# Kernel tuning notes

Hardware: AMD Instinct MI355X
Metric: run time of the kernel (lower is better)

The kernel has to match this reference:

```python
import jax, jax.numpy as jnp
import numpy as np

P_DIMS = [512, 256, 128]
K_DIMS = [256, 256, 256]
NT = 65536


def setup_inputs() -> dict:
    key = jax.random.key(0)
    ks = jax.random.split(key, 8 * len(P_DIMS))
    inp = {}
    ki = 0
    for i, (p, k) in enumerate(zip(P_DIMS, K_DIMS)):
        inp[f"x{i}"] = jax.random.normal(ks[ki], (NT, p), jnp.float32); ki += 1
        inp[f"alpha{i}"] = jax.random.normal(ks[ki], (1, k), jnp.float32); ki += 1
        inp[f"beta{i}"] = jax.random.normal(ks[ki], (k, p), jnp.float32) * 0.05; ki += 1
        inp[f"sig{i}"] = jax.random.normal(ks[ki], (1, k), jnp.float32); ki += 1
        inp[f"eta{i}"] = jax.random.normal(ks[ki], (1, k), jnp.float32); ki += 1
        inp[f"gam{i}"] = jax.random.normal(ks[ki], (k, 1), jnp.float32) * 0.03; ki += 1
        inp[f"w{i}"] = jax.random.normal(ks[ki], (k, p), jnp.float32); ki += 1
        inp[f"disc{i}"] = jnp.array([3.0], jnp.float32); ki += 1
    return inp


def _source(x, alpha, beta, sig, eta, gam, w, disc):
    # x: (nt,p); w,beta: (k,p); alpha,sig,eta: (1,k); gam: (k,1); disc: (1,)
    h = eta ** 2                                           # (1,k)
    d2 = (jnp.sum(x * x, axis=1, keepdims=True)
          - 2.0 * (x @ w.T)
          + jnp.sum(w * w, axis=1)[None, :])
    a = jnp.exp(-(gam[:, 0] ** 2)[None, :] * d2)           # (nt,k)
    ah = a * h                                             # a * H
    hx = jnp.sum(ah, axis=1)                               # (nt,)
    mu = x @ beta.T + alpha                                # (nt,k)
    mux = jnp.sum(mu * ah, axis=1) / hx
    sig2x = jnp.sum((sig ** 2) * (ah ** 2), axis=1) / (hx * hx)
    hx_dc = hx * jax.nn.sigmoid(disc[0])
    return mux, sig2x, hx, hx_dc


def reference(x0, alpha0, beta0, sig0, eta0, gam0, w0, disc0,
              x1, alpha1, beta1, sig1, eta1, gam1, w1, disc1,
              x2, alpha2, beta2, sig2, eta2, gam2, w2, disc2):
    srcs = [
        (x0, alpha0, beta0, sig0, eta0, gam0, w0, disc0),
        (x1, alpha1, beta1, sig1, eta1, gam1, w1, disc1),
        (x2, alpha2, beta2, sig2, eta2, gam2, w2, disc2),
    ]
    outs = [_source(*s) for s in srcs]  # fixed small loop over sources
    mux_t = jnp.stack([o[0] for o in outs])     # (S,nt)
    sig2x_t = jnp.stack([o[1] for o in outs])
    hx_t = jnp.stack([o[2] for o in outs])
    hx_dc = jnp.stack([o[3] for o in outs])
    denom = jnp.sum(hx_dc, axis=0)
    mux_comb = jnp.sum(mux_t * hx_dc, axis=0) / denom
    sig2x_comb = jnp.sum(sig2x_t * hx_dc ** 2, axis=0) / (denom ** 2)
    mux_final = jnp.concatenate([mux_t, mux_comb[None]], axis=0)      # (S+1,nt)
    sig2x_final = jnp.concatenate([sig2x_t, sig2x_comb[None]], axis=0)
    hx_final = jnp.concatenate([hx_t, denom[None]], axis=0)
    return (mux_final, sig2x_final, hx_final)
```

## Files before the change

kernel.cpp:

```cpp
#include <hip/hip_runtime.h>
#include <hip/hip_bf16.h>

typedef __attribute__((ext_vector_type(8))) short short8;
typedef __attribute__((ext_vector_type(4))) float f32x4;

#define NT 65536

__device__ __forceinline__ unsigned short f2bf(float f) {
    union { float f; unsigned int u; } v; v.f = f;
    unsigned int u = v.u;
    unsigned int r = (u + 0x7fffu + ((u >> 16) & 1u)) >> 16;
    return (unsigned short)r;
}

__device__ __forceinline__ unsigned int cvt_pk_bf16(float lo, float hi) {
    unsigned int r;
    asm("v_cvt_pk_bf16_f32 %0, %1, %2" : "=v"(r) : "v"(lo), "v"(hi));
    return r;
}

#define LGKM0()  asm volatile("s_waitcnt lgkmcnt(0)" ::: "memory")
#define BAR()    __builtin_amdgcn_s_barrier()
#define SB0()    __builtin_amdgcn_sched_barrier(0)

__global__ void prep_kernel(const float* __restrict__ w0, const float* __restrict__ b0,
                            const float* __restrict__ a0, const float* __restrict__ s0,
                            const float* __restrict__ e0, const float* __restrict__ g0,
                            const float* __restrict__ w1, const float* __restrict__ b1,
                            const float* __restrict__ a1, const float* __restrict__ s1,
                            const float* __restrict__ e1, const float* __restrict__ g1,
                            const float* __restrict__ w2, const float* __restrict__ b2,
                            const float* __restrict__ a2, const float* __restrict__ s2,
                            const float* __restrict__ e2, const float* __restrict__ g2,
                            unsigned short* __restrict__ bc, float* __restrict__ prmAll) {
    __shared__ float red[2];
    const int bx = blockIdx.x;
    const int s = bx >> 9;
    const int n = bx & 511;
    const int P = 512 >> s;
    const float* w   = (s == 0) ? w0 : ((s == 1) ? w1 : w2);
    const float* bet = (s == 0) ? b0 : ((s == 1) ? b1 : b2);
    const float* alp = (s == 0) ? a0 : ((s == 1) ? a1 : a2);
    const float* sig = (s == 0) ? s0 : ((s == 1) ? s1 : s2);
    const float* eta = (s == 0) ? e0 : ((s == 1) ? e1 : e2);
    const float* gam = (s == 0) ? g0 : ((s == 1) ? g1 : g2);
    unsigned short* dstb = bc + ((s == 0) ? 0 : ((s == 1) ? (512 * 512) : (512 * 512 + 512 * 256)));
    float* prm = prmAll + 1280 * s;

    const int tid = threadIdx.x;
    const int k16 = n >> 5;
    const int typ = (n >> 4) & 1;
    const int k = k16 * 16 + (n & 15);
    const bool isw = (typ == 0);
    const float* src = (isw ? w : bet) + (size_t)k * P;
    unsigned short* dst = dstb + (size_t)n * P;
    float ss = 0.f;
    for (int c = tid; c < P; c += 128) {
        float f = src[c];
        dst[c] = f2bf(f);
        if (isw) ss += f * f;
    }
#pragma unroll
    for (int m = 1; m < 64; m <<= 1) ss += __shfl_xor(ss, m);
    if ((tid & 63) == 0) red[tid >> 6] = ss;
    __syncthreads();
    if (isw && tid == 0) prm[k] = red[0] + red[1];
    if (n == 0) {
        for (int kk = tid; kk < 256; kk += 128) {
            float g = gam[kk], e = eta[kk];
            prm[256 + kk]  = g * g;
            prm[512 + kk]  = e * e;
            prm[768 + kk]  = alp[kk];
            prm[1024 + kk] = sig[kk] * sig[kk];
        }
    }
}

template<int P>
__global__ __launch_bounds__(256, 3)
void fused_src(const float* __restrict__ x, const unsigned short* __restrict__ Bc,
               const float* __restrict__ prm, float* __restrict__ pwsS) {
    constexpr int NK = P / 32;
    __shared__ unsigned short Bs[4][128 * 32];
    __shared__ unsigned short Xs[2][128 * 32];
    __shared__ float xn2[128];

    const int b = blockIdx.x;
    const int xt = (b >> 5) * 8 + (b & 7);
    const int pt = (b >> 3) & 3;

    const int tid = threadIdx.x, lane = tid & 63, wv = tid >> 6;
    const int wp = wv >> 1, wx = wv & 1;
    const int l15 = lane & 15, l4 = lane >> 4;

    const int srow = tid >> 1, shalf = tid & 1;
    const float* xbase = x + (size_t)(xt * 128 + srow) * P + shalf * 16;

    f32x4 acc[4][4];
#pragma unroll
    for (int pf = 0; pf < 4; pf++)
#pragma unroll
        for (int xf = 0; xf < 4; xf++) acc[pf][xf] = (f32x4){0.f, 0.f, 0.f, 0.f};

    float4 xr[4][4];
    float ss = 0.f;

    auto gloadB = [&](int nb, int t) {
#pragma unroll
        for (int i = 0; i < 2; i++) {
            const int u = i * 256 + tid;
            const int row = u >> 2;
            const int sl = (u & 3) ^ ((row >> 1) & 3);
            const unsigned short* src = Bc + (size_t)(pt * 128 + row) * P + t * 32 + sl * 8;
            __builtin_amdgcn_global_load_lds((const __attribute__((address_space(1))) void*)src,
                (__attribute__((address_space(3))) void*)&Bs[nb][(i * 256 + wv * 64) * 8], 16, 0, 0);
        }
    };
    auto loadX = [&](float4* xrs, int t) {
#pragma unroll
        for (int i = 0; i < 4; i++) xrs[i] = *(const float4*)(xbase + t * 32 + i * 4);
    };
    auto cvtWrite = [&](const float4* xrs, int xb) {
        const int sw = (srow >> 1) & 3;
#pragma unroll
        for (int hh = 0; hh < 2; hh++) {
            float4 q0 = xrs[2 * hh], q1 = xrs[2 * hh + 1];
            ss += q0.x*q0.x + q0.y*q0.y + q0.z*q0.z + q0.w*q0.w
                + q1.x*q1.x + q1.y*q1.y + q1.z*q1.z + q1.w*q1.w;
            uint4 pk = { cvt_pk_bf16(q0.x, q0.y), cvt_pk_bf16(q0.z, q0.w),
                         cvt_pk_bf16(q1.x, q1.y), cvt_pk_bf16(q1.z, q1.w) };
            const int phys = (shalf * 2 + hh) ^ sw;
            *(uint4*)(&Xs[xb][srow * 32 + phys * 8]) = pk;
        }
    };
    auto compute = [&](int bb, int xb) {
        short8 af[4], bf[4];
#pragma unroll
        for (int pf = 0; pf < 4; pf++) {
            const int row = 64 * wp + 16 * pf + l15;
            af[pf] = *(const short8*)(&Bs[bb][row * 32 + ((l4 ^ ((row >> 1) & 3)) << 3)]);
        }
#pragma unroll
        for (int xf = 0; xf < 4; xf++) {
            const int row = 64 * wx + 16 * xf + l15;
            bf[xf] = *(const short8*)(&Xs[xb][row * 32 + ((l4 ^ ((row >> 1) & 3)) << 3)]);
        }
#pragma unroll
        for (int pf = 0; pf < 4; pf++)
#pragma unroll
            for (int xf = 0; xf < 4; xf++)
                acc[pf][xf] = __builtin_amdgcn_mfma_f32_16x16x32_bf16(af[pf], bf[xf], acc[pf][xf], 0, 0, 0);
    };

#pragma unroll
    for (int d = 0; d < 3; d++) {
        if (d < NK) {
            gloadB(d, d); SB0();
            loadX(xr[d], d); SB0();
        }
    }
    cvtWrite(xr[0], 0);
    LGKM0(); SB0(); BAR(); SB0();

#pragma unroll
    for (int t = 0; t < NK; t++) {
        if (t + 3 < NK) {
            gloadB((t + 3) & 3, t + 3); SB0();
            loadX(xr[(t + 3) & 3], t + 3); SB0();
        }
        if (t + 1 < NK) {
            cvtWrite(xr[(t + 1) & 3], (t + 1) & 1);
        }
        LGKM0(); SB0(); BAR(); SB0();
        compute(t & 3, t & 1);
        SB0(); BAR(); SB0();
    }

    ss += __shfl_xor(ss, 1);
    if (shalf == 0) xn2[srow] = ss;
    __syncthreads();

    const int kb0 = (pt * 4 + 2 * wp) * 16 + 4 * l4;
    f32x4 wn2[2], g2[2], hv[2], alv[2], s2v[2];
#pragma unroll
    for (int K = 0; K < 2; K++) {
        const int kk = kb0 + 16 * K;
        wn2[K] = *(const f32x4*)(prm + kk);
        g2[K]  = *(const f32x4*)(prm + 256 + kk);
        hv[K]  = *(const f32x4*)(prm + 512 + kk);
        alv[K] = *(const f32x4*)(prm + 768 + kk);
        s2v[K] = *(const f32x4*)(prm + 1024 + kk);
    }
    float (*part)[128][3] = (float (*)[128][3])(&Bs[0][0]);
#pragma unroll
    for (int xf = 0; xf < 4; xf++) {
        const int xrow = 64 * wx + 16 * xf + l15;
        const float xv = xn2[xrow];
        float hs = 0.f, ms = 0.f, gs = 0.f;
#pragma unroll
        for (int K = 0; K < 2; K++) {
#pragma unroll
            for (int j = 0; j < 4; j++) {
                const float aw = acc[2 * K][xf][j];
                const float ab = acc[2 * K + 1][xf][j];
                const float d2 = xv - 2.f * aw + wn2[K][j];
                const float a  = __expf(-g2[K][j] * d2);
                const float ah = a * hv[K][j];
                hs += ah;
                ms += (ab + alv[K][j]) * ah;
                gs += s2v[K][j] * ah * ah;
            }
        }
        hs += __shfl_xor(hs, 16); hs += __shfl_xor(hs, 32);
        ms += __shfl_xor(ms, 16); ms += __shfl_xor(ms, 32);
        gs += __shfl_xor(gs, 16); gs += __shfl_xor(gs, 32);
        if (l4 == 0) {
            part[wp][xrow][0] = hs;
            part[wp][xrow][1] = ms;
            part[wp][xrow][2] = gs;
        }
    }
    __syncthreads();
    if (tid < 128) {
        const int gr = xt * 128 + tid;
#pragma unroll
        for (int v = 0; v < 3; v++)
            pwsS[(size_t)(pt * 3 + v) * NT + gr] = part[0][tid][v] + part[1][tid][v];
    }
}

__global__ void combine_kernel(const float* __restrict__ pws,
                               const float* __restrict__ d0, const float* __restrict__ d1,
                               const float* __restrict__ d2, float* __restrict__ out) {
    const int t = blockIdx.x * 256 + threadIdx.x;
    float mux[3], s2x[3], hx[3];
#pragma unroll
    for (int s = 0; s < 3; s++) {
        const float* bbase = pws + (size_t)s * 12 * NT;
        float hh = 0.f, mm = 0.f, gg = 0.f;
#pragma unroll
        for (int pt = 0; pt < 4; pt++) {
            hh += bbase[(size_t)(pt * 3 + 0) * NT + t];
            mm += bbase[(size_t)(pt * 3 + 1) * NT + t];
            gg += bbase[(size_t)(pt * 3 + 2) * NT + t];
        }
        mux[s] = mm / hh; s2x[s] = gg / (hh * hh); hx[s] = hh;
        out[(size_t)s * NT + t]       = mux[s];
        out[(size_t)(4 + s) * NT + t] = s2x[s];
        out[(size_t)(8 + s) * NT + t] = hh;
    }
    const float sd0 = 1.f / (1.f + __expf(-d0[0]));
    const float sd1 = 1.f / (1.f + __expf(-d1[0]));
    const float sd2 = 1.f / (1.f + __expf(-d2[0]));
    const float c0 = hx[0] * sd0, c1 = hx[1] * sd1, c2 = hx[2] * sd2;
    const float den = c0 + c1 + c2;
    const float muc = mux[0] * c0 + mux[1] * c1 + mux[2] * c2;
    const float sgc = s2x[0] * c0 * c0 + s2x[1] * c1 * c1 + s2x[2] * c2 * c2;
    out[(size_t)3 * NT + t]  = muc / den;
    out[(size_t)7 * NT + t]  = sgc / (den * den);
    out[(size_t)11 * NT + t] = den;
}

extern "C" void kernel_launch(void* const* d_in, const int* in_sizes, int n_in,
                              void* d_out, int out_size, void* d_ws, size_t ws_size,
                              hipStream_t stream) {
    const float* x0 = (const float*)d_in[0];
    const float* x1 = (const float*)d_in[8];
    const float* x2 = (const float*)d_in[16];

    unsigned short* bc = (unsigned short*)d_ws;
    float* prmAll = (float*)((char*)d_ws + 917504);
    float* pws    = (float*)((char*)d_ws + 917504 + 15360);
    float* out = (float*)d_out;

    prep_kernel<<<1536, 128, 0, stream>>>(
        (const float*)d_in[6],  (const float*)d_in[2],  (const float*)d_in[1],
        (const float*)d_in[3],  (const float*)d_in[4],  (const float*)d_in[5],
        (const float*)d_in[14], (const float*)d_in[10], (const float*)d_in[9],
        (const float*)d_in[11], (const float*)d_in[12], (const float*)d_in[13],
        (const float*)d_in[22], (const float*)d_in[18], (const float*)d_in[17],
        (const float*)d_in[19], (const float*)d_in[20], (const float*)d_in[21],
        bc, prmAll);

    const size_t bcoff1 = 512 * 512, bcoff2 = 512 * 512 + 512 * 256;
    fused_src<512><<<2048, 256, 0, stream>>>(x0, bc,          prmAll,        pws);
    fused_src<256><<<2048, 256, 0, stream>>>(x1, bc + bcoff1, prmAll + 1280, pws + (size_t)12 * NT);
    fused_src<128><<<2048, 256, 0, stream>>>(x2, bc + bcoff2, prmAll + 2560, pws + (size_t)24 * NT);
    combine_kernel<<<256, 256, 0, stream>>>(pws, (const float*)d_in[7], (const float*)d_in[15],
                                            (const float*)d_in[23], out);
}
```

Before: 126.1 us.

## Stream fp32 X via LDS DMA and load B fragments directly into registers

The fused source kernel stops staging the bf16 weight tile in LDS. Each wave now loads its A fragments straight from global memory into double-buffered registers. X is copied as fp32 into a triple-buffered, XOR-swizzled LDS ring with global_load_lds, then converted to bf16 and squared at fragment-read time rather than through a separate register staging pass. The loop keeps one barrier per step and uses vmcnt waits, aiming to cut register pressure, LDS writes and barriers. In exchange, LDS traffic per X element doubles, conversion work is repeated by both wp waves, and correctness depends on the vmcnt counts matching the number of outstanding loads.

```diff
diff --git a/kernel.cpp b/kernel.cpp
--- a/kernel.cpp
+++ b/kernel.cpp
@@ -19,9 +19,11 @@
     return r;
 }
 
-#define LGKM0()  asm volatile("s_waitcnt lgkmcnt(0)" ::: "memory")
-#define BAR()    __builtin_amdgcn_s_barrier()
-#define SB0()    __builtin_amdgcn_sched_barrier(0)
+#define VMCNT12() asm volatile("s_waitcnt vmcnt(12)" ::: "memory")
+#define VMCNT8()  asm volatile("s_waitcnt vmcnt(8)" ::: "memory")
+#define VMCNT0()  asm volatile("s_waitcnt vmcnt(0)" ::: "memory")
+#define BAR()     __builtin_amdgcn_s_barrier()
+#define SB0()     __builtin_amdgcn_sched_barrier(0)
 
 __global__ void prep_kernel(const float* __restrict__ w0, const float* __restrict__ b0,
                             const float* __restrict__ a0, const float* __restrict__ s0,
@@ -81,8 +83,7 @@
 void fused_src(const float* __restrict__ x, const unsigned short* __restrict__ Bc,
                const float* __restrict__ prm, float* __restrict__ pwsS) {
     constexpr int NK = P / 32;
-    __shared__ unsigned short Bs[4][128 * 32];
-    __shared__ unsigned short Xs[2][128 * 32];
+    __shared__ float Xs[3][128 * 32];
     __shared__ float xn2[128];
 
     const int b = blockIdx.x;
@@ -93,91 +94,86 @@
     const int wp = wv >> 1, wx = wv & 1;
     const int l15 = lane & 15, l4 = lane >> 4;
 
-    const int srow = tid >> 1, shalf = tid & 1;
-    const float* xbase = x + (size_t)(xt * 128 + srow) * P + shalf * 16;
-
     f32x4 acc[4][4];
 #pragma unroll
     for (int pf = 0; pf < 4; pf++)
 #pragma unroll
         for (int xf = 0; xf < 4; xf++) acc[pf][xf] = (f32x4){0.f, 0.f, 0.f, 0.f};
 
-    float4 xr[4][4];
-    float ss = 0.f;
-
-    auto gloadB = [&](int nb, int t) {
-#pragma unroll
-        for (int i = 0; i < 2; i++) {
+    const unsigned short* afp[4];
+#pragma unroll
+    for (int pf = 0; pf < 4; pf++)
+        afp[pf] = Bc + (size_t)(pt * 128 + 64 * wp + 16 * pf + l15) * P + l4 * 8;
+
+    short8 bg[2][4];
+    float ssx[4] = {0.f, 0.f, 0.f, 0.f};
+
+    auto bgload = [&](int set, int t) {
+#pragma unroll
+        for (int pf = 0; pf < 4; pf++)
+            bg[set][pf] = *(const short8*)(afp[pf] + t * 32);
+    };
+    auto dmaX = [&](int slot, int t) {
+#pragma unroll
+        for (int i = 0; i < 4; i++) {
             const int u = i * 256 + tid;
-            const int row = u >> 2;
-            const int sl = (u & 3) ^ ((row >> 1) & 3);
-            const unsigned short* src = Bc + (size_t)(pt * 128 + row) * P + t * 32 + sl * 8;
+            const int row = u >> 3;
+            const int c = u & 7;
+            const float* src = x + (size_t)(xt * 128 + row) * P + t * 32 + ((c ^ (row & 7)) << 2);
             __builtin_amdgcn_global_load_lds((const __attribute__((address_space(1))) void*)src,
-                (__attribute__((address_space(3))) void*)&Bs[nb][(i * 256 + wv * 64) * 8], 16, 0, 0);
+                (__attribute__((address_space(3))) void*)((char*)&Xs[slot][0] + u * 16), 16, 0, 0);
         }
     };
-    auto loadX = [&](float4* xrs, int t) {
-#pragma unroll
-        for (int i = 0; i < 4; i++) xrs[i] = *(const float4*)(xbase + t * 32 + i * 4);
-    };
-    auto cvtWrite = [&](const float4* xrs, int xb) {
-        const int sw = (srow >> 1) & 3;
-#pragma unroll
-        for (int hh = 0; hh < 2; hh++) {
-            float4 q0 = xrs[2 * hh], q1 = xrs[2 * hh + 1];
-            ss += q0.x*q0.x + q0.y*q0.y + q0.z*q0.z + q0.w*q0.w
-                + q1.x*q1.x + q1.y*q1.y + q1.z*q1.z + q1.w*q1.w;
+    auto compute = [&](int slot, int set) {
+        short8 bf[4];
+#pragma unroll
+        for (int xf = 0; xf < 4; xf++) {
+            const int row = 64 * wx + 16 * xf + l15;
+            const float* base = &Xs[slot][row * 32];
+            const int sw = row & 7;
+            float4 q0 = *(const float4*)(base + (((l4 * 2) ^ sw) << 2));
+            float4 q1 = *(const float4*)(base + (((l4 * 2 + 1) ^ sw) << 2));
+            if (wp == 0)
+                ssx[xf] += q0.x*q0.x + q0.y*q0.y + q0.z*q0.z + q0.w*q0.w
+                         + q1.x*q1.x + q1.y*q1.y + q1.z*q1.z + q1.w*q1.w;
             uint4 pk = { cvt_pk_bf16(q0.x, q0.y), cvt_pk_bf16(q0.z, q0.w),
                          cvt_pk_bf16(q1.x, q1.y), cvt_pk_bf16(q1.z, q1.w) };
-            const int phys = (shalf * 2 + hh) ^ sw;
-            *(uint4*)(&Xs[xb][srow * 32 + phys * 8]) = pk;
-        }
+            bf[xf] = *(short8*)&pk;
+        }
+#pragma unroll
+        for (int pf = 0; pf < 4; pf++)
+#pragma unroll
+            for (int xf = 0; xf < 4; xf++)
+                acc[pf][xf] = __builtin_amdgcn_mfma_f32_16x16x32_bf16(bg[set][pf], bf[xf], acc[pf][xf], 0, 0, 0);
     };
-    auto compute = [&](int bb, int xb) {
-        short8 af[4], bf[4];
-#pragma unroll
-        for (int pf = 0; pf < 4; pf++) {
-            const int row = 64 * wp + 16 * pf + l15;
-            af[pf] = *(const short8*)(&Bs[bb][row * 32 + ((l4 ^ ((row >> 1) & 3)) << 3)]);
-        }
+
+    bgload(0, 0); SB0();
+    dmaX(0, 0);
+    if (NK > 1) dmaX(1, 1);
+    SB0();
+
+#pragma unroll
+    for (int t = 0; t < NK; t++) {
+        BAR(); SB0();
+        if (t + 1 < NK) { bgload((t + 1) & 1, t + 1); SB0(); }
+        if (t + 2 < NK) { dmaX((t + 2) % 3, t + 2); SB0(); }
+        if (t + 2 < NK)      { VMCNT12(); }
+        else if (t + 1 < NK) { VMCNT8();  }
+        else                 { VMCNT0();  }
+        SB0();
+        compute(t % 3, t & 1);
+        SB0();
+    }
+
+    if (wp == 0) {
 #pragma unroll
         for (int xf = 0; xf < 4; xf++) {
-            const int row = 64 * wx + 16 * xf + l15;
-            bf[xf] = *(const short8*)(&Xs[xb][row * 32 + ((l4 ^ ((row >> 1) & 3)) << 3)]);
-        }
-#pragma unroll
-        for (int pf = 0; pf < 4; pf++)
-#pragma unroll
-            for (int xf = 0; xf < 4; xf++)
-                acc[pf][xf] = __builtin_amdgcn_mfma_f32_16x16x32_bf16(af[pf], bf[xf], acc[pf][xf], 0, 0, 0);
-    };
-
-#pragma unroll
-    for (int d = 0; d < 3; d++) {
-        if (d < NK) {
-            gloadB(d, d); SB0();
-            loadX(xr[d], d); SB0();
-        }
-    }
-    cvtWrite(xr[0], 0);
-    LGKM0(); SB0(); BAR(); SB0();
-
-#pragma unroll
-    for (int t = 0; t < NK; t++) {
-        if (t + 3 < NK) {
-            gloadB((t + 3) & 3, t + 3); SB0();
-            loadX(xr[(t + 3) & 3], t + 3); SB0();
-        }
-        if (t + 1 < NK) {
-            cvtWrite(xr[(t + 1) & 3], (t + 1) & 1);
-        }
-        LGKM0(); SB0(); BAR(); SB0();
-        compute(t & 3, t & 1);
-        SB0(); BAR(); SB0();
-    }
-
-    ss += __shfl_xor(ss, 1);
-    if (shalf == 0) xn2[srow] = ss;
+            float v = ssx[xf];
+            v += __shfl_xor(v, 16);
+            v += __shfl_xor(v, 32);
+            if (l4 == 0) xn2[64 * wx + 16 * xf + l15] = v;
+        }
+    }
     __syncthreads();
 
     const int kb0 = (pt * 4 + 2 * wp) * 16 + 4 * l4;
@@ -191,7 +187,7 @@
         alv[K] = *(const f32x4*)(prm + 768 + kk);
         s2v[K] = *(const f32x4*)(prm + 1024 + kk);
     }
-    float (*part)[128][3] = (float (*)[128][3])(&Bs[0][0]);
+    float (*part)[128][3] = (float (*)[128][3])(&Xs[0][0]);
 #pragma unroll
     for (int xf = 0; xf < 4; xf++) {
         const int xrow = 64 * wx + 16 * xf + l15;
```

Result: slower. 224.9 us (+78.5%).

## Keep weight fragments in registers and stream x tiles through persistent blocks

Applied to the files above, without the earlier changes.

Each block of eight waves now holds its slice of the weight/beta matrix (32 output columns per wave, half of the 512 combined columns per block) resident in registers for the whole kernel. It then loops over eight 32-row x tiles, double-buffering x through LDS. This removes the repeated per-block streaming of B into LDS and cuts x re-reads from four column-tile passes to two, so the partial-sum workspace and the combine reads shrink too. The cost is much higher register pressure for large P (64 short8 fragments at P=512), small 32-row MFMA tiles with low reuse per LDS read, and a barrier-heavy epilogue every tile.

```diff
diff --git a/kernel.cpp b/kernel.cpp
--- a/kernel.cpp
+++ b/kernel.cpp
@@ -77,155 +77,130 @@
 }
 
 template<int P>
-__global__ __launch_bounds__(256, 3)
+__global__ __launch_bounds__(512, 2)
 void fused_src(const float* __restrict__ x, const unsigned short* __restrict__ Bc,
                const float* __restrict__ prm, float* __restrict__ pwsS) {
-    constexpr int NK = P / 32;
-    __shared__ unsigned short Bs[4][128 * 32];
-    __shared__ unsigned short Xs[2][128 * 32];
-    __shared__ float xn2[128];
+    constexpr int KSW = P / 32;
+    constexpr int CPT = P / 64;
+    constexpr int QPT = (CPT / 2 > 0) ? CPT / 2 : 1;
+    constexpr int T = 8;
+
+    __shared__ unsigned short Xs[2][32 * P];
+    __shared__ float xn2[2][32];
+    __shared__ float part[8][32][3];
 
     const int b = blockIdx.x;
-    const int xt = (b >> 5) * 8 + (b & 7);
-    const int pt = (b >> 3) & 3;
+    const int h = b >> 8;
+    const int rg = b & 255;
+    const int rowbase = rg * 256;
 
     const int tid = threadIdx.x, lane = tid & 63, wv = tid >> 6;
-    const int wp = wv >> 1, wx = wv & 1;
     const int l15 = lane & 15, l4 = lane >> 4;
-
-    const int srow = tid >> 1, shalf = tid & 1;
-    const float* xbase = x + (size_t)(xt * 128 + srow) * P + shalf * 16;
-
-    f32x4 acc[4][4];
-#pragma unroll
-    for (int pf = 0; pf < 4; pf++)
-#pragma unroll
-        for (int xf = 0; xf < 4; xf++) acc[pf][xf] = (f32x4){0.f, 0.f, 0.f, 0.f};
-
-    float4 xr[4][4];
-    float ss = 0.f;
-
-    auto gloadB = [&](int nb, int t) {
-#pragma unroll
-        for (int i = 0; i < 2; i++) {
-            const int u = i * 256 + tid;
-            const int row = u >> 2;
-            const int sl = (u & 3) ^ ((row >> 1) & 3);
-            const unsigned short* src = Bc + (size_t)(pt * 128 + row) * P + t * 32 + sl * 8;
-            __builtin_amdgcn_global_load_lds((const __attribute__((address_space(1))) void*)src,
-                (__attribute__((address_space(3))) void*)&Bs[nb][(i * 256 + wv * 64) * 8], 16, 0, 0);
-        }
+    const int k16 = h * 8 + wv;
+
+    const int srow = tid >> 4;
+    const int sc = tid & 15;
+    const float* xth = x + (size_t)(rowbase + srow) * P + sc * (P / 16);
+
+    short8 Bf0[KSW], Bf1[KSW];
+#pragma unroll
+    for (int ks = 0; ks < KSW; ks++) {
+        Bf0[ks] = *(const short8*)(Bc + (size_t)(k16 * 32 + l15) * P + ks * 32 + l4 * 8);
+        Bf1[ks] = *(const short8*)(Bc + (size_t)(k16 * 32 + 16 + l15) * P + ks * 32 + l4 * 8);
+    }
+
+    f32x4 acc00 = {0,0,0,0}, acc01 = {0,0,0,0}, acc10 = {0,0,0,0}, acc11 = {0,0,0,0};
+    float4 xr[CPT];
+
+    auto issueX = [&](int t) {
+#pragma unroll
+        for (int j = 0; j < CPT; j++)
+            xr[j] = *(const float4*)(xth + (size_t)t * 32 * P + j * 4);
     };
-    auto loadX = [&](float4* xrs, int t) {
-#pragma unroll
-        for (int i = 0; i < 4; i++) xrs[i] = *(const float4*)(xbase + t * 32 + i * 4);
+    auto cvtWrite = [&](int bufp) {
+        float s = 0.f;
+#pragma unroll
+        for (int q = 0; q < QPT; q++) {
+            float4 a = xr[2 * q], c = xr[2 * q + 1];
+            s += a.x*a.x + a.y*a.y + a.z*a.z + a.w*a.w
+               + c.x*c.x + c.y*c.y + c.z*c.z + c.w*c.w;
+            uint4 pk = { cvt_pk_bf16(a.x, a.y), cvt_pk_bf16(a.z, a.w),
+                         cvt_pk_bf16(c.x, c.y), cvt_pk_bf16(c.z, c.w) };
+            const int m = sc * QPT + q;
+            *(uint4*)(&Xs[bufp][srow * P + ((m ^ (srow & 7)) << 3)]) = pk;
+        }
+        s += __shfl_xor(s, 1); s += __shfl_xor(s, 2);
+        s += __shfl_xor(s, 4); s += __shfl_xor(s, 8);
+        if (sc == 0) xn2[bufp][srow] = s;
     };
-    auto cvtWrite = [&](const float4* xrs, int xb) {
-        const int sw = (srow >> 1) & 3;
-#pragma unroll
-        for (int hh = 0; hh < 2; hh++) {
-            float4 q0 = xrs[2 * hh], q1 = xrs[2 * hh + 1];
-            ss += q0.x*q0.x + q0.y*q0.y + q0.z*q0.z + q0.w*q0.w
-                + q1.x*q1.x + q1.y*q1.y + q1.z*q1.z + q1.w*q1.w;
-            uint4 pk = { cvt_pk_bf16(q0.x, q0.y), cvt_pk_bf16(q0.z, q0.w),
-                         cvt_pk_bf16(q1.x, q1.y), cvt_pk_bf16(q1.z, q1.w) };
-            const int phys = (shalf * 2 + hh) ^ sw;
-            *(uint4*)(&Xs[xb][srow * 32 + phys * 8]) = pk;
+    auto compute = [&](int bufp) {
+#pragma unroll
+        for (int ks = 0; ks < KSW; ks++) {
+            const int m = (ks * 4 + l4) ^ (l15 & 7);
+            short8 xf0 = *(const short8*)(&Xs[bufp][l15 * P + (m << 3)]);
+            short8 xf1 = *(const short8*)(&Xs[bufp][(16 + l15) * P + (m << 3)]);
+            acc00 = __builtin_amdgcn_mfma_f32_16x16x32_bf16(Bf0[ks], xf0, acc00, 0, 0, 0);
+            acc10 = __builtin_amdgcn_mfma_f32_16x16x32_bf16(Bf1[ks], xf0, acc10, 0, 0, 0);
+            acc01 = __builtin_amdgcn_mfma_f32_16x16x32_bf16(Bf0[ks], xf1, acc01, 0, 0, 0);
+            acc11 = __builtin_amdgcn_mfma_f32_16x16x32_bf16(Bf1[ks], xf1, acc11, 0, 0, 0);
         }
     };
-    auto compute = [&](int bb, int xb) {
-        short8 af[4], bf[4];
-#pragma unroll
-        for (int pf = 0; pf < 4; pf++) {
-            const int row = 64 * wp + 16 * pf + l15;
-            af[pf] = *(const short8*)(&Bs[bb][row * 32 + ((l4 ^ ((row >> 1) & 3)) << 3)]);
-        }
-#pragma unroll
-        for (int xf = 0; xf < 4; xf++) {
-            const int row = 64 * wx + 16 * xf + l15;
-            bf[xf] = *(const short8*)(&Xs[xb][row * 32 + ((l4 ^ ((row >> 1) & 3)) << 3)]);
-        }
-#pragma unroll
-        for (int pf = 0; pf < 4; pf++)
-#pragma unroll
-            for (int xf = 0; xf < 4; xf++)
-                acc[pf][xf] = __builtin_amdgcn_mfma_f32_16x16x32_bf16(af[pf], bf[xf], acc[pf][xf], 0, 0, 0);
-    };
-
-#pragma unroll
-    for (int d = 0; d < 3; d++) {
-        if (d < NK) {
-            gloadB(d, d); SB0();
-            loadX(xr[d], d); SB0();
-        }
-    }
-    cvtWrite(xr[0], 0);
-    LGKM0(); SB0(); BAR(); SB0();
-
-#pragma unroll
-    for (int t = 0; t < NK; t++) {
-        if (t + 3 < NK) {
-            gloadB((t + 3) & 3, t + 3); SB0();
-            loadX(xr[(t + 3) & 3], t + 3); SB0();
-        }
-        if (t + 1 < NK) {
-            cvtWrite(xr[(t + 1) & 3], (t + 1) & 1);
-        }
+
+    issueX(0); SB0();
+    cvtWrite(0); SB0();
+    issueX(1); SB0();
+
+#pragma unroll
+    for (int t = 0; t < T; t++) {
         LGKM0(); SB0(); BAR(); SB0();
-        compute(t & 3, t & 1);
-        SB0(); BAR(); SB0();
-    }
-
-    ss += __shfl_xor(ss, 1);
-    if (shalf == 0) xn2[srow] = ss;
-    __syncthreads();
-
-    const int kb0 = (pt * 4 + 2 * wp) * 16 + 4 * l4;
-    f32x4 wn2[2], g2[2], hv[2], alv[2], s2v[2];
-#pragma unroll
-    for (int K = 0; K < 2; K++) {
-        const int kk = kb0 + 16 * K;
-        wn2[K] = *(const f32x4*)(prm + kk);
-        g2[K]  = *(const f32x4*)(prm + 256 + kk);
-        hv[K]  = *(const f32x4*)(prm + 512 + kk);
-        alv[K] = *(const f32x4*)(prm + 768 + kk);
-        s2v[K] = *(const f32x4*)(prm + 1024 + kk);
-    }
-    float (*part)[128][3] = (float (*)[128][3])(&Bs[0][0]);
-#pragma unroll
-    for (int xf = 0; xf < 4; xf++) {
-        const int xrow = 64 * wx + 16 * xf + l15;
-        const float xv = xn2[xrow];
-        float hs = 0.f, ms = 0.f, gs = 0.f;
-#pragma unroll
-        for (int K = 0; K < 2; K++) {
-#pragma unroll
-            for (int j = 0; j < 4; j++) {
-                const float aw = acc[2 * K][xf][j];
-                const float ab = acc[2 * K + 1][xf][j];
-                const float d2 = xv - 2.f * aw + wn2[K][j];
-                const float a  = __expf(-g2[K][j] * d2);
-                const float ah = a * hv[K][j];
-                hs += ah;
-                ms += (ab + alv[K][j]) * ah;
-                gs += s2v[K][j] * ah * ah;
+        if (t + 1 < T) { cvtWrite((t + 1) & 1); SB0(); }
+        if (t + 2 < T) { issueX(t + 2); SB0(); }
+        compute(t & 1);
+        SB0();
+
+        {
+            const int kb = k16 * 16 + 4 * l4;
+            const f32x4 wn2 = *(const f32x4*)(prm + kb);
+            const f32x4 g2  = *(const f32x4*)(prm + 256 + kb);
+            const f32x4 hv  = *(const f32x4*)(prm + 512 + kb);
+            const f32x4 alv = *(const f32x4*)(prm + 768 + kb);
+            const f32x4 s2v = *(const f32x4*)(prm + 1024 + kb);
+#pragma unroll
+            for (int xf = 0; xf < 2; xf++) {
+                const int xrow = xf * 16 + l15;
+                const float xv = xn2[t & 1][xrow];
+                const f32x4 aw = xf ? acc01 : acc00;
+                const f32x4 ab = xf ? acc11 : acc10;
+                float hs = 0.f, ms = 0.f, gs = 0.f;
+#pragma unroll
+                for (int j = 0; j < 4; j++) {
+                    const float d2 = xv - 2.f * aw[j] + wn2[j];
+                    const float e  = __expf(-g2[j] * d2);
+                    const float ah = e * hv[j];
+                    hs += ah;
+                    ms += (ab[j] + alv[j]) * ah;
+                    gs += s2v[j] * ah * ah;
+                }
+                hs += __shfl_xor(hs, 16); hs += __shfl_xor(hs, 32);
+                ms += __shfl_xor(ms, 16); ms += __shfl_xor(ms, 32);
+                gs += __shfl_xor(gs, 16); gs += __shfl_xor(gs, 32);
+                if (l4 == 0) {
+                    part[wv][xrow][0] = hs;
+                    part[wv][xrow][1] = ms;
+                    part[wv][xrow][2] = gs;
+                }
             }
         }
-        hs += __shfl_xor(hs, 16); hs += __shfl_xor(hs, 32);
-        ms += __shfl_xor(ms, 16); ms += __shfl_xor(ms, 32);
-        gs += __shfl_xor(gs, 16); gs += __shfl_xor(gs, 32);
-        if (l4 == 0) {
-            part[wp][xrow][0] = hs;
-            part[wp][xrow][1] = ms;
-            part[wp][xrow][2] = gs;
-        }
-    }
-    __syncthreads();
-    if (tid < 128) {
-        const int gr = xt * 128 + tid;
-#pragma unroll
-        for (int v = 0; v < 3; v++)
-            pwsS[(size_t)(pt * 3 + v) * NT + gr] = part[0][tid][v] + part[1][tid][v];
+        LGKM0(); SB0(); BAR(); SB0();
+        if (tid < 96) {
+            const int v = tid >> 5, r = tid & 31;
+            float s = 0.f;
+#pragma unroll
+            for (int w8 = 0; w8 < 8; w8++) s += part[w8][r][v];
+            pwsS[(size_t)(h * 3 + v) * NT + rowbase + t * 32 + r] = s;
+        }
+        acc00 = (f32x4){0,0,0,0}; acc01 = (f32x4){0,0,0,0};
+        acc10 = (f32x4){0,0,0,0}; acc11 = (f32x4){0,0,0,0};
     }
 }
 
@@ -236,14 +211,10 @@
     float mux[3], s2x[3], hx[3];
 #pragma unroll
     for (int s = 0; s < 3; s++) {
-        const float* bbase = pws + (size_t)s * 12 * NT;
-        float hh = 0.f, mm = 0.f, gg = 0.f;
-#pragma unroll
-        for (int pt = 0; pt < 4; pt++) {
-            hh += bbase[(size_t)(pt * 3 + 0) * NT + t];
-            mm += bbase[(size_t)(pt * 3 + 1) * NT + t];
-            gg += bbase[(size_t)(pt * 3 + 2) * NT + t];
-        }
+        const float* bb = pws + (size_t)s * 6 * NT;
+        const float hh = bb[t] + bb[(size_t)3 * NT + t];
+        const float mm = bb[(size_t)1 * NT + t] + bb[(size_t)4 * NT + t];
+        const float gg = bb[(size_t)2 * NT + t] + bb[(size_t)5 * NT + t];
         mux[s] = mm / hh; s2x[s] = gg / (hh * hh); hx[s] = hh;
         out[(size_t)s * NT + t]       = mux[s];
         out[(size_t)(4 + s) * NT + t] = s2x[s];
@@ -283,9 +254,9 @@
         bc, prmAll);
 
     const size_t bcoff1 = 512 * 512, bcoff2 = 512 * 512 + 512 * 256;
-    fused_src<512><<<2048, 256, 0, stream>>>(x0, bc,          prmAll,        pws);
-    fused_src<256><<<2048, 256, 0, stream>>>(x1, bc + bcoff1, prmAll + 1280, pws + (size_t)12 * NT);
-    fused_src<128><<<2048, 256, 0, stream>>>(x2, bc + bcoff2, prmAll + 2560, pws + (size_t)24 * NT);
+    fused_src<512><<<512, 512, 0, stream>>>(x0, bc,          prmAll,        pws);
+    fused_src<256><<<512, 512, 0, stream>>>(x1, bc + bcoff1, prmAll + 1280, pws + (size_t)6 * NT);
+    fused_src<128><<<512, 512, 0, stream>>>(x2, bc + bcoff2, prmAll + 2560, pws + (size_t)12 * NT);
     combine_kernel<<<256, 256, 0, stream>>>(pws, (const float*)d_in[7], (const float*)d_in[15],
                                             (const float*)d_in[23], out);
 }
```

Measured after the change: 148.7 us. 18.0% more time.

## Add persistent register-resident-B kernel for the largest source, halving x re-reads

Applied to the files above, without the earlier changes.

Replaces the tiled kernel for source 0 (P=512) with a persistent 512-thread kernel. It keeps its half of the combined w/beta bf16 fragments in registers and streams 64-row x tiles through double-buffered, swizzled LDS, prefetching the next tile from global memory during the MFMA loop. The k dimension is split into two halves instead of four column tiles, so each x row is read twice rather than four times. The combine kernel is changed to the new two-partial layout. The cost is heavy register pressure, about 128KB of LDS per block, and only one block per CU, which could limit latency hiding.

```diff
diff --git a/kernel.cpp b/kernel.cpp
--- a/kernel.cpp
+++ b/kernel.cpp
@@ -18,10 +18,6 @@
     asm("v_cvt_pk_bf16_f32 %0, %1, %2" : "=v"(r) : "v"(lo), "v"(hi));
     return r;
 }
-
-#define LGKM0()  asm volatile("s_waitcnt lgkmcnt(0)" ::: "memory")
-#define BAR()    __builtin_amdgcn_s_barrier()
-#define SB0()    __builtin_amdgcn_sched_barrier(0)
 
 __global__ void prep_kernel(const float* __restrict__ w0, const float* __restrict__ b0,
                             const float* __restrict__ a0, const float* __restrict__ s0,
@@ -77,9 +73,171 @@
 }
 
 template<int P>
+__global__ __launch_bounds__(512, 2)
+void fused_s0(const float* __restrict__ x, const unsigned short* __restrict__ Bc,
+              const float* __restrict__ prm, float* __restrict__ pws) {
+    constexpr int KS  = P / 32;
+    constexpr int IST = P / 64;
+    constexpr int WIN = (P == 256) ? 4 : 2;
+    __shared__ unsigned short As[2][64 * P];
+    __shared__ float part[8][64][3];
+    __shared__ float xn2s[2][64];
+
+    const int bx = blockIdx.x;
+    const int h  = bx & 1;
+    const int rg = bx >> 1;
+    const int tid = threadIdx.x, lane = tid & 63, wv = tid >> 6;
+    const int l15 = lane & 15, l4 = lane >> 4;
+    const int k16 = h * 8 + wv;
+
+    short8 Bf[2][KS];
+#pragma unroll
+    for (int st = 0; st < 2; st++)
+#pragma unroll
+        for (int ks = 0; ks < KS; ks++)
+            Bf[st][ks] = *(const short8*)(Bc + (size_t)(k16 * 32 + st * 16 + l15) * P + ks * 32 + l4 * 8);
+
+    const int kb = k16 * 16 + 4 * l4;
+    const f32x4 wn2 = *(const f32x4*)(prm + kb);
+    const f32x4 g2  = *(const f32x4*)(prm + 256 + kb);
+    const f32x4 hv  = *(const f32x4*)(prm + 512 + kb);
+    const f32x4 alv = *(const f32x4*)(prm + 768 + kb);
+    const f32x4 s2v = *(const f32x4*)(prm + 1024 + kb);
+
+    const int srow = tid >> 3;
+    const int ssl0 = tid & 7;
+
+    {
+        const int row0 = rg * 64;
+        float4 pa[IST], pb[IST];
+#pragma unroll
+        for (int i = 0; i < IST; i++) {
+            const float* gp = x + (size_t)(row0 + srow) * P + (ssl0 + 8 * i) * 8;
+            pa[i] = *(const float4*)(gp);
+            pb[i] = *(const float4*)(gp + 4);
+        }
+        float ssacc = 0.f;
+#pragma unroll
+        for (int i = 0; i < IST; i++) {
+            float4 a0 = pa[i], a1 = pb[i];
+            ssacc += a0.x*a0.x + a0.y*a0.y + a0.z*a0.z + a0.w*a0.w
+                   + a1.x*a1.x + a1.y*a1.y + a1.z*a1.z + a1.w*a1.w;
+            uint4 pk = { cvt_pk_bf16(a0.x, a0.y), cvt_pk_bf16(a0.z, a0.w),
+                         cvt_pk_bf16(a1.x, a1.y), cvt_pk_bf16(a1.z, a1.w) };
+            const int slot = ssl0 + 8 * i;
+            *(uint4*)(&As[0][srow * P + ((slot ^ (srow & 7)) << 3)]) = pk;
+        }
+        ssacc += __shfl_xor(ssacc, 1);
+        ssacc += __shfl_xor(ssacc, 2);
+        ssacc += __shfl_xor(ssacc, 4);
+        if (ssl0 == 0) xn2s[0][srow] = ssacc;
+    }
+    __syncthreads();
+
+    int buf = 0;
+    for (int tt = 0; tt < 8; tt++) {
+        const int tile = rg + 128 * tt;
+        const int row0 = tile * 64;
+        const bool more = (tt < 7);
+        const int nrow0 = (tile + 128) * 64;
+
+        f32x4 acc[2][4];
+#pragma unroll
+        for (int st = 0; st < 2; st++)
+#pragma unroll
+            for (int rf = 0; rf < 4; rf++) acc[st][rf] = (f32x4){0.f, 0.f, 0.f, 0.f};
+
+        float4 gfa[WIN], gfb[WIN];
+        float ssacc = 0.f;
+
+#pragma unroll
+        for (int ks = 0; ks < KS; ks++) {
+            if (more && ks >= WIN && (ks - WIN) < IST) {
+                const int i = ks - WIN;
+                float4 a0 = gfa[i % WIN], a1 = gfb[i % WIN];
+                ssacc += a0.x*a0.x + a0.y*a0.y + a0.z*a0.z + a0.w*a0.w
+                       + a1.x*a1.x + a1.y*a1.y + a1.z*a1.z + a1.w*a1.w;
+                uint4 pk = { cvt_pk_bf16(a0.x, a0.y), cvt_pk_bf16(a0.z, a0.w),
+                             cvt_pk_bf16(a1.x, a1.y), cvt_pk_bf16(a1.z, a1.w) };
+                const int slot = ssl0 + 8 * i;
+                *(uint4*)(&As[buf ^ 1][srow * P + ((slot ^ (srow & 7)) << 3)]) = pk;
+            }
+            if (more && ks < IST) {
+                const float* gp = x + (size_t)(nrow0 + srow) * P + (ssl0 + 8 * ks) * 8;
+                gfa[ks % WIN] = *(const float4*)(gp);
+                gfb[ks % WIN] = *(const float4*)(gp + 4);
+            }
+            short8 af[4];
+#pragma unroll
+            for (int rf = 0; rf < 4; rf++) {
+                const int row = 16 * rf + l15;
+                af[rf] = *(const short8*)(&As[buf][row * P + (((ks * 4 + l4) ^ (row & 7)) << 3)]);
+            }
+#pragma unroll
+            for (int rf = 0; rf < 4; rf++) {
+                acc[0][rf] = __builtin_amdgcn_mfma_f32_16x16x32_bf16(Bf[0][ks], af[rf], acc[0][rf], 0, 0, 0);
+                acc[1][rf] = __builtin_amdgcn_mfma_f32_16x16x32_bf16(Bf[1][ks], af[rf], acc[1][rf], 0, 0, 0);
+            }
+        }
+
+        if (more) {
+#pragma unroll
+            for (int i = (KS - WIN < 0 ? 0 : KS - WIN); i < IST; i++) {
+                float4 a0 = gfa[i % WIN], a1 = gfb[i % WIN];
+                ssacc += a0.x*a0.x + a0.y*a0.y + a0.z*a0.z + a0.w*a0.w
+                       + a1.x*a1.x + a1.y*a1.y + a1.z*a1.z + a1.w*a1.w;
+                uint4 pk = { cvt_pk_bf16(a0.x, a0.y), cvt_pk_bf16(a0.z, a0.w),
+                             cvt_pk_bf16(a1.x, a1.y), cvt_pk_bf16(a1.z, a1.w) };
+                const int slot = ssl0 + 8 * i;
+                *(uint4*)(&As[buf ^ 1][srow * P + ((slot ^ (srow & 7)) << 3)]) = pk;
+            }
+            ssacc += __shfl_xor(ssacc, 1);
+            ssacc += __shfl_xor(ssacc, 2);
+            ssacc += __shfl_xor(ssacc, 4);
+            if (ssl0 == 0) xn2s[buf ^ 1][srow] = ssacc;
+        }
+        __syncthreads();
+
+#pragma unroll
+        for (int rf = 0; rf < 4; rf++) {
+            const int row = 16 * rf + l15;
+            const float xv = xn2s[buf][row];
+            float hs = 0.f, ms = 0.f, gs = 0.f;
+#pragma unroll
+            for (int j = 0; j < 4; j++) {
+                float d2 = xv - 2.f * acc[0][rf][j] + wn2[j];
+                float a  = __expf(-g2[j] * d2);
+                float ah = a * hv[j];
+                hs += ah;
+                ms += (acc[1][rf][j] + alv[j]) * ah;
+                gs += s2v[j] * ah * ah;
+            }
+            hs += __shfl_xor(hs, 16); hs += __shfl_xor(hs, 32);
+            ms += __shfl_xor(ms, 16); ms += __shfl_xor(ms, 32);
+            gs += __shfl_xor(gs, 16); gs += __shfl_xor(gs, 32);
+            if (l4 == 0) { part[wv][row][0] = hs; part[wv][row][1] = ms; part[wv][row][2] = gs; }
+        }
+        __syncthreads();
+        if (tid < 192) {
+            const int v = tid >> 6, r = tid & 63;
+            float sum = 0.f;
+#pragma unroll
+            for (int w8 = 0; w8 < 8; w8++) sum += part[w8][r][v];
+            pws[(size_t)(h * 3 + v) * NT + row0 + r] = sum;
+        }
+        __syncthreads();
+        buf ^= 1;
+    }
+}
+
+#define LGKM0()  asm volatile("s_waitcnt lgkmcnt(0)" ::: "memory")
+#define BAR()    __builtin_amdgcn_s_barrier()
+#define SB0()    __builtin_amdgcn_sched_barrier(0)
+
+template<int P>
 __global__ __launch_bounds__(256, 3)
-void fused_src(const float* __restrict__ x, const unsigned short* __restrict__ Bc,
-               const float* __restrict__ prm, float* __restrict__ pwsS) {
+void fused_small(const float* __restrict__ x, const unsigned short* __restrict__ Bc,
+                 const float* __restrict__ prm, float* __restrict__ pwsS) {
     constexpr int NK = P / 32;
     __shared__ unsigned short Bs[4][128 * 32];
     __shared__ unsigned short Xs[2][128 * 32];
@@ -234,20 +392,30 @@
                                const float* __restrict__ d2, float* __restrict__ out) {
     const int t = blockIdx.x * 256 + threadIdx.x;
     float mux[3], s2x[3], hx[3];
+    {
+        const float* b = pws;
+        const float hh = b[t] + b[(size_t)3 * NT + t];
+        const float mm = b[(size_t)1 * NT + t] + b[(size_t)4 * NT + t];
+        const float gg = b[(size_t)2 * NT + t] + b[(size_t)5 * NT + t];
+        mux[0] = mm / hh; s2x[0] = gg / (hh * hh); hx[0] = hh;
+    }
+#pragma unroll
+    for (int s = 1; s < 3; s++) {
+        const float* b = pws + (size_t)(6 + (s - 1) * 12) * NT;
+        float hh = 0.f, mm = 0.f, gg = 0.f;
+#pragma unroll
+        for (int pt = 0; pt < 4; pt++) {
+            hh += b[(size_t)(pt * 3 + 0) * NT + t];
+            mm += b[(size_t)(pt * 3 + 1) * NT + t];
+            gg += b[(size_t)(pt * 3 + 2) * NT + t];
+        }
+        mux[s] = mm / hh; s2x[s] = gg / (hh * hh); hx[s] = hh;
+    }
 #pragma unroll
     for (int s = 0; s < 3; s++) {
-        const float* bbase = pws + (size_t)s * 12 * NT;
-        float hh = 0.f, mm = 0.f, gg = 0.f;
-#pragma unroll
-        for (int pt = 0; pt < 4; pt++) {
-            hh += bbase[(size_t)(pt * 3 + 0) * NT + t];
-            mm += bbase[(size_t)(pt * 3 + 1) * NT + t];
-            gg += bbase[(size_t)(pt * 3 + 2) * NT + t];
-        }
-        mux[s] = mm / hh; s2x[s] = gg / (hh * hh); hx[s] = hh;
         out[(size_t)s * NT + t]       = mux[s];
         out[(size_t)(4 + s) * NT + t] = s2x[s];
-        out[(size_t)(8 + s) * NT + t] = hh;
+        out[(size_t)(8 + s) * NT + t] = hx[s];
     }
     const float sd0 = 1.f / (1.f + __expf(-d0[0]));
     const float sd1 = 1.f / (1.f + __expf(-d1[0]));
@@ -283,9 +451,9 @@
         bc, prmAll);
 
     const size_t bcoff1 = 512 * 512, bcoff2 = 512 * 512 + 512 * 256;
-    fused_src<512><<<2048, 256, 0, stream>>>(x0, bc,          prmAll,        pws);
-    fused_src<256><<<2048, 256, 0, stream>>>(x1, bc + bcoff1, prmAll + 1280, pws + (size_t)12 * NT);
-    fused_src<128><<<2048, 256, 0, stream>>>(x2, bc + bcoff2, prmAll + 2560, pws + (size_t)24 * NT);
+    fused_s0<512><<<256, 512, 0, stream>>>(x0, bc, prmAll, pws);
+    fused_small<256><<<2048, 256, 0, stream>>>(x1, bc + bcoff1, prmAll + 1280, pws + (size_t)6 * NT);
+    fused_small<128><<<2048, 256, 0, stream>>>(x2, bc + bcoff2, prmAll + 2560, pws + (size_t)18 * NT);
     combine_kernel<<<256, 256, 0, stream>>>(pws, (const float*)d_in[7], (const float*)d_in[15],
                                             (const float*)d_in[23], out);
 }
```

Result: slower. 129.5 us (+2.8%).
